# Optimization experiments

Measured on AMD Instinct MI355X. Metric: run time of the kernel, lower is better.

## Reference

```python
import jax, jax.numpy as jnp
import numpy as np

VOC_SIZE = 32768
DIM = 512
NUM_TOPK = 64
BATCH = 4096


def setup_inputs() -> dict:
    key = jax.random.key(0)
    ks = jax.random.split(key, 8)
    lim = 1.0 / np.sqrt(DIM)  # kaiming_uniform(a=sqrt(5)) on [V, d] -> U(-1/sqrt(d), 1/sqrt(d))
    x = jax.random.normal(ks[0], (BATCH, DIM), dtype=jnp.float32)
    codebook = jax.random.uniform(ks[1], (VOC_SIZE, DIM), dtype=jnp.float32, minval=-lim, maxval=lim)
    Wq = jax.random.uniform(ks[2], (DIM, DIM), dtype=jnp.float32, minval=-lim, maxval=lim)
    bq = jax.random.uniform(ks[3], (DIM,), dtype=jnp.float32, minval=-lim, maxval=lim)
    Wk = jax.random.uniform(ks[4], (DIM, DIM), dtype=jnp.float32, minval=-lim, maxval=lim)
    bk = jax.random.uniform(ks[5], (DIM,), dtype=jnp.float32, minval=-lim, maxval=lim)
    Wv = jax.random.uniform(ks[6], (DIM, DIM), dtype=jnp.float32, minval=-lim, maxval=lim)
    bv = jax.random.uniform(ks[7], (DIM,), dtype=jnp.float32, minval=-lim, maxval=lim)
    return {"x": x, "codebook": codebook, "Wq": Wq, "bq": bq,
            "Wk": Wk, "bk": bk, "Wv": Wv, "bv": bv}


def reference(x, codebook, Wq, bq, Wk, bk, Wv, bv):
    # projections (torch Linear with weight stored pre-transposed as [in, out])
    q = x @ Wq + bq              # [B, d]
    k = codebook @ Wk + bk       # [V, d]
    v = codebook @ Wv + bv       # [V, d]

    dots = jnp.einsum('bd,kd->bk', q, k)              # [B, V]
    top, _ = jax.lax.top_k(dots, NUM_TOPK)            # [B, num_topk]
    thresh = top[..., -1:]                            # k-th largest value per row
    mask_value = -jnp.finfo(dots.dtype).max
    dots = jnp.where(dots < thresh, mask_value, dots)
    attn = jax.nn.softmax(dots, axis=-1)              # [B, V]
    out = jnp.einsum('bk,kd->bd', attn, v)            # [B, d]
    return out
```

## Files before the change

### kernel.cpp

```cpp
#include <hip/hip_runtime.h>
#include <cstdint>

#define VOC   32768
#define DIM   512
#define TOPK  64
#define BATCH 4096

#define KSIG     2.45f
#define EPS_SEL  0.012f
#define CAND_CAP 512
#define RES_CAP  256
#define FCAP     1024

typedef unsigned short u16;
typedef __attribute__((ext_vector_type(8))) short bf16x8;
typedef __attribute__((ext_vector_type(4))) float f32x4;

__device__ __forceinline__ u16 f2bf(float f) {
    unsigned u = __float_as_uint(f);
    unsigned r = (u + 0x7FFFu + ((u >> 16) & 1u)) >> 16;
    return (u16)r;
}
__device__ __forceinline__ float bf2f(u16 h) {
    return __uint_as_float(((unsigned)h) << 16);
}
__device__ __forceinline__ unsigned enc16(u16 h) {
    return (h & 0x8000u) ? (unsigned)((u16)~h) : (unsigned)(h | 0x8000u);
}
__device__ __forceinline__ float dec16(unsigned s16) {
    u16 h = (s16 & 0x8000u) ? (u16)(s16 ^ 0x8000u) : (u16)(~s16);
    return bf2f(h);
}

__device__ __forceinline__ void async16(const void* g, void* l) {
    __builtin_amdgcn_global_load_lds(
        (const __attribute__((address_space(1))) void*)g,
        (__attribute__((address_space(3))) void*)l, 16, 0, 0);
}

template <bool BT, bool F64ACC>
__global__ __launch_bounds__(256)
void gemm64(const float* __restrict__ A, const float* __restrict__ B,
            const float* __restrict__ bias, float* __restrict__ C,
            int M, int N, int K)
{
    const int KS = 16;
    __shared__ float As[KS][68];
    __shared__ float Bs[KS][64];

    const int tid = threadIdx.x;
    const int m0 = blockIdx.y * 64;
    const int n0 = blockIdx.x * 64;
    const int ty = tid >> 4;
    const int tx = tid & 15;

    float acc[4][4];
    double acc64[4][4];
#pragma unroll
    for (int i = 0; i < 4; i++)
#pragma unroll
        for (int j = 0; j < 4; j++) { acc[i][j] = 0.f; if (F64ACC) acc64[i][j] = 0.0; }

    for (int kt = 0; kt < K; kt += KS) {
        {
            int row = tid >> 2, kq = tid & 3;
            const float4 av = *(const float4*)(A + (size_t)(m0 + row) * K + kt + kq * 4);
            As[kq * 4 + 0][row] = av.x;
            As[kq * 4 + 1][row] = av.y;
            As[kq * 4 + 2][row] = av.z;
            As[kq * 4 + 3][row] = av.w;
        }
        if (!BT) {
            int krow = tid >> 4, nq = tid & 15;
            *(float4*)&Bs[krow][nq * 4] =
                *(const float4*)(B + (size_t)(kt + krow) * N + n0 + nq * 4);
        } else {
            int nrow = tid >> 2, kq = tid & 3;
            const float4 bv = *(const float4*)(B + (size_t)(n0 + nrow) * K + kt + kq * 4);
            Bs[kq * 4 + 0][nrow] = bv.x;
            Bs[kq * 4 + 1][nrow] = bv.y;
            Bs[kq * 4 + 2][nrow] = bv.z;
            Bs[kq * 4 + 3][nrow] = bv.w;
        }
        __syncthreads();

#pragma unroll
        for (int kk = 0; kk < KS; kk++) {
            float4 a = *(const float4*)&As[kk][ty * 4];
            float4 b = *(const float4*)&Bs[kk][tx * 4];
            float av[4] = {a.x, a.y, a.z, a.w};
            float bv[4] = {b.x, b.y, b.z, b.w};
#pragma unroll
            for (int i = 0; i < 4; i++)
#pragma unroll
                for (int j = 0; j < 4; j++)
                    acc[i][j] += av[i] * bv[j];
        }
        __syncthreads();
        if (F64ACC) {
#pragma unroll
            for (int i = 0; i < 4; i++)
#pragma unroll
                for (int j = 0; j < 4; j++) { acc64[i][j] += (double)acc[i][j]; acc[i][j] = 0.f; }
        }
    }

    float4 bb = make_float4(0.f, 0.f, 0.f, 0.f);
    if (bias) bb = *(const float4*)(bias + n0 + tx * 4);
#pragma unroll
    for (int i = 0; i < 4; i++) {
        float4 o;
        o.x = (F64ACC ? (float)acc64[i][0] : acc[i][0]) + bb.x;
        o.y = (F64ACC ? (float)acc64[i][1] : acc[i][1]) + bb.y;
        o.z = (F64ACC ? (float)acc64[i][2] : acc[i][2]) + bb.z;
        o.w = (F64ACC ? (float)acc64[i][3] : acc[i][3]) + bb.w;
        *(float4*)(C + (size_t)(m0 + ty * 4 + i) * N + n0 + tx * 4) = o;
    }
}

__global__ __launch_bounds__(256)
void bias_fold(const float* __restrict__ bq, const float* __restrict__ Wk,
               float* __restrict__ bqk)
{
    const int lane = threadIdx.x & 63, wave = threadIdx.x >> 6;
    const int j = blockIdx.x * 4 + wave;
    const float* wr = Wk + (size_t)j * DIM + lane * 8;
    const float* bp = bq + lane * 8;
    double s = 0.0;
#pragma unroll
    for (int t = 0; t < 8; t++) s += (double)bp[t] * (double)wr[t];
#pragma unroll
    for (int off = 32; off > 0; off >>= 1) s += __shfl_down(s, off);
    if (lane == 0) bqk[j] = (float)s;
}

__global__ void zero_ws(unsigned* __restrict__ p, int n)
{
    int i = blockIdx.x * 256 + threadIdx.x;
    if (i < n) p[i] = 0u;
}

__global__ __launch_bounds__(256)
void cbar_accum(const float* __restrict__ cb, float* __restrict__ cbarsum)
{
    const int tid = threadIdx.x;
    const int r0 = blockIdx.x * 128;
    float s0 = 0.f, s1 = 0.f;
    for (int r = 0; r < 128; r++) {
        const float* rp = cb + (size_t)(r0 + r) * DIM;
        s0 += rp[tid];
        s1 += rp[tid + 256];
    }
    atomicAdd(&cbarsum[tid], s0);
    atomicAdd(&cbarsum[tid + 256], s1);
}

__global__ __launch_bounds__(256)
void rowstats(const float* __restrict__ q2, const float* __restrict__ cbarsum,
              float* __restrict__ trow, float* __restrict__ sigrow)
{
    const int tid = threadIdx.x, lane = tid & 63, wave = tid >> 6;
    const int row = blockIdx.x * 4 + wave;
    const float* qp = q2 + (size_t)row * DIM + lane * 8;
    float4 a0 = *(const float4*)qp, a1 = *(const float4*)(qp + 4);
    const float* cp = cbarsum + lane * 8;
    float4 c0 = *(const float4*)cp, c1 = *(const float4*)(cp + 4);
    float mu = a0.x*c0.x + a0.y*c0.y + a0.z*c0.z + a0.w*c0.w
             + a1.x*c1.x + a1.y*c1.y + a1.z*c1.z + a1.w*c1.w;
    float nr = a0.x*a0.x + a0.y*a0.y + a0.z*a0.z + a0.w*a0.w
             + a1.x*a1.x + a1.y*a1.y + a1.z*a1.z + a1.w*a1.w;
#pragma unroll
    for (int off = 32; off > 0; off >>= 1) {
        mu += __shfl_down(mu, off);
        nr += __shfl_down(nr, off);
    }
    if (lane == 0) {
        mu *= (1.f / VOC);
        float sig = sqrtf(nr * (1.f / 1536.f));
        trow[row] = mu + KSIG * sig;
        sigrow[row] = sig;
    }
}

__global__ __launch_bounds__(256)
void pack_rows(const float* __restrict__ src, u16* __restrict__ hi,
               u16* __restrict__ lo, int R, int log2R)
{
    int idx = blockIdx.x * 256 + threadIdx.x;
    int c8  = idx >> log2R;
    int row = idx & (R - 1);
    const float* sp = src + (size_t)row * DIM + c8 * 8;
    float xv[8];
    *(float4*)&xv[0] = *(const float4*)sp;
    *(float4*)&xv[4] = *(const float4*)(sp + 4);
    int ks = c8 >> 2, ch = c8 & 3;
    size_t ob = ((size_t)(ks * 4 + ch) * R + row) * 8;
    u16 h[8], l[8];
#pragma unroll
    for (int j = 0; j < 8; j++) {
        h[j] = f2bf(xv[j]);
        l[j] = f2bf(xv[j] - bf2f(h[j]));
    }
    *(uint4*)(hi + ob) = *(const uint4*)h;
    if (lo) *(uint4*)(lo + ob) = *(const uint4*)l;
}

__global__ __launch_bounds__(256)
void pack_bT(const float* __restrict__ W, u16* __restrict__ hi, u16* __restrict__ lo)
{
    int idx = blockIdx.x * 256 + threadIdx.x;
    int n  = idx & (DIM - 1);
    int c8 = idx >> 9;
    int ks = c8 >> 2, ch = c8 & 3;
    size_t ob = ((size_t)(ks * 4 + ch) * DIM + n) * 8;
    u16 h[8], l[8];
#pragma unroll
    for (int j = 0; j < 8; j++) {
        float x = W[(size_t)(c8 * 8 + j) * DIM + n];
        h[j] = f2bf(x);
        l[j] = f2bf(x - bf2f(h[j]));
    }
    *(uint4*)(hi + ob) = *(const uint4*)h;
    *(uint4*)(lo + ob) = *(const uint4*)l;
}

__global__ __launch_bounds__(256, 4)
void mfma_dots(const u16* __restrict__ Ah, const u16* __restrict__ Bh,
               const float* __restrict__ trow, unsigned* __restrict__ candBuf,
               unsigned* __restrict__ counters)
{
    __shared__ u16 lds[4 * 4096];

    const int tid  = threadIdx.x;
    const int lane = tid & 63;
    const int wave = tid >> 6;
    const int wm = wave >> 1, wn = wave & 1;
    const int lr = lane & 15;
    const int q  = lane >> 4;

    const int L   = blockIdx.x;
    const int xcd = L & 7;
    const int j   = L >> 3;
    const int m0  = (xcd * 4 + (j & 3)) * 128;
    const int n0  = (j >> 2) * 128;

    u16* wlds = &lds[wave * 4096];

#define AISSUE(ks, st)                                                         \
    { _Pragma("unroll")                                                        \
      for (int ch_ = 0; ch_ < 4; ch_++) {                                      \
          const u16* gp_ = Ah + ((size_t)((ks) * 4 + ch_) * BATCH              \
                                 + m0 + wm * 64 + lane) * 8;                   \
          async16(gp_, &wlds[(st) * 2048 + ch_ * 512 + lane * 8]);             \
      } }

#define BPTR(nt, ks) ((const bf16x8*)(Bh + ((size_t)((ks) * 4 + q) * VOC       \
                                            + n0 + wn * 64 + (nt) * 16 + lr) * 8))

    f32x4 acc[4][4] = {};
    bf16x8 bb[2][4];

    AISSUE(0, 0)
#pragma unroll
    for (int nt = 0; nt < 4; nt++) bb[0][nt] = *BPTR(nt, 0);

#pragma unroll
    for (int s = 0; s < 16; s++) {
        const int st = s & 1;
        __builtin_amdgcn_s_waitcnt(0x0F70);

        bf16x8 ah[4];
#pragma unroll
        for (int mt = 0; mt < 4; mt++)
            ah[mt] = *(const bf16x8*)&wlds[st * 2048 + q * 512 + (mt * 16 + lr) * 8];

        __builtin_amdgcn_sched_barrier(0);
        __builtin_amdgcn_s_waitcnt(0xC47F);
        if (s < 15) AISSUE(s + 1, st ^ 1)

        __builtin_amdgcn_s_setprio(1);
#pragma unroll
        for (int nt = 0; nt < 4; nt++) {
            if (s < 15) bb[st ^ 1][nt] = *BPTR(nt, s + 1);
#pragma unroll
            for (int mt = 0; mt < 4; mt++)
                acc[mt][nt] = __builtin_amdgcn_mfma_f32_16x16x32_bf16(
                    ah[mt], bb[st][nt], acc[mt][nt], 0, 0, 0);
        }
        __builtin_amdgcn_s_setprio(0);
    }
#undef AISSUE
#undef BPTR

#pragma unroll
    for (int mt = 0; mt < 4; mt++) {
#pragma unroll
        for (int r = 0; r < 4; r++) {
            int rowg = m0 + wm * 64 + mt * 16 + q * 4 + r;
            float tr = trow[rowg];
#pragma unroll
            for (int nt = 0; nt < 4; nt++) {
                float val = acc[mt][nt][r];
                if (val >= tr) {
                    unsigned slot = atomicAdd(&counters[rowg], 1u);
                    if (slot < CAND_CAP) {
                        unsigned s16 = enc16(f2bf(val));
                        candBuf[(size_t)rowg * CAND_CAP + slot] =
                            (s16 << 16) | (unsigned)(n0 + wn * 64 + nt * 16 + lr);
                    }
                }
            }
        }
    }
}

__global__ __launch_bounds__(256, 2)
void mfma_out(const u16* __restrict__ Ah, const u16* __restrict__ Al,
              const u16* __restrict__ Bh, const u16* __restrict__ Bl,
              const float* __restrict__ bias, float* __restrict__ Cout, int Ma)
{
    __shared__ u16 lds[2 * 16384];

    const int tid  = threadIdx.x;
    const int lane = tid & 63;
    const int wave = tid >> 6;
    const int wm = wave >> 1, wn = wave & 1;
    const int m0 = blockIdx.y * 128, n0 = blockIdx.x * 128;
    const int lr = lane & 15;
    const int q  = lane >> 4;

    f32x4 acc[4][4] = {};
    const u16* garr[4] = {Ah, Bh, Al, Bl};
    const int a = wave;
    const u16* src = garr[a];
    const bool isA = (a == 0 || a == 2);
    const int rb = isA ? m0 : n0;
    const size_t R = isA ? (size_t)Ma : (size_t)DIM;

#define VISSUE(ks, b)                                                         \
    {                                                                         \
        _Pragma("unroll")                                                     \
        for (int i_ = 0; i_ < 8; i_++) {                                      \
            const u16* gp_ = src + ((size_t)((ks) * 4 + (i_ >> 1)) * R + rb   \
                                    + (i_ & 1) * 64 + lane) * 8;              \
            async16(gp_, &lds[(b) * 16384 + a * 4096 + i_ * 512 + lane * 8]); \
        }                                                                     \
    }

    VISSUE(0, 0)

    for (int ks = 0; ks < 16; ks++) {
        __syncthreads();
        if (ks < 15) VISSUE(ks + 1, (ks + 1) & 1)
        const u16* base = &lds[(ks & 1) * 16384];

        bf16x8 ah[4], al[4];
#pragma unroll
        for (int mt = 0; mt < 4; mt++) {
            int row = wm * 64 + mt * 16 + lr;
            ah[mt] = *(const bf16x8*)&base[0 * 4096 + q * 1024 + row * 8];
            al[mt] = *(const bf16x8*)&base[2 * 4096 + q * 1024 + row * 8];
        }
#pragma unroll
        for (int nt = 0; nt < 4; nt++) {
            int col = wn * 64 + nt * 16 + lr;
            bf16x8 bh = *(const bf16x8*)&base[1 * 4096 + q * 1024 + col * 8];
            bf16x8 bl = *(const bf16x8*)&base[3 * 4096 + q * 1024 + col * 8];
#pragma unroll
            for (int mt = 0; mt < 4; mt++) {
                acc[mt][nt] = __builtin_amdgcn_mfma_f32_16x16x32_bf16(ah[mt], bh, acc[mt][nt], 0, 0, 0);
                acc[mt][nt] = __builtin_amdgcn_mfma_f32_16x16x32_bf16(ah[mt], bl, acc[mt][nt], 0, 0, 0);
                acc[mt][nt] = __builtin_amdgcn_mfma_f32_16x16x32_bf16(al[mt], bh, acc[mt][nt], 0, 0, 0);
            }
        }
    }
#undef VISSUE

#pragma unroll
    for (int mt = 0; mt < 4; mt++)
#pragma unroll
        for (int nt = 0; nt < 4; nt++) {
            int col = n0 + wn * 64 + nt * 16 + lr;
            float bb = bias[col];
#pragma unroll
            for (int r = 0; r < 4; r++) {
                int rowg = m0 + wm * 64 + mt * 16 + q * 4 + r;
                Cout[(size_t)rowg * DIM + col] = acc[mt][nt][r] + bb;
            }
        }
}

__global__ __launch_bounds__(256)
void select6(const unsigned* __restrict__ candBuf, const unsigned* __restrict__ counters,
             const float* __restrict__ trow, const float* __restrict__ q2,
             const float* __restrict__ codebook, float* __restrict__ y,
             unsigned* __restrict__ flags)
{
    __shared__ unsigned recs[CAND_CAP];
    __shared__ unsigned list[RES_CAP];
    __shared__ unsigned hist[256];
    __shared__ unsigned long long keys[RES_CAP];
    __shared__ float q2s[DIM];
    __shared__ float wArr[RES_CAP];
    __shared__ float redf[256];
    __shared__ unsigned redu[256];
    __shared__ unsigned s_R;
    __shared__ unsigned s_b1, s_rem, s_thr;

    const int tid  = threadIdx.x;
    const int lane = tid & 63;
    const int wave = tid >> 6;
    const int row  = blockIdx.x;

    const unsigned cnt = counters[row];
    if (cnt < TOPK || cnt > CAND_CAP) {
        if (tid == 0) flags[row] = 1u;
        return;
    }
    for (int i = tid; i < DIM; i += 256) q2s[i] = q2[(size_t)row * DIM + i];
    for (int i = tid; i < CAND_CAP; i += 256)
        recs[i] = (i < (int)cnt) ? candBuf[(size_t)row * CAND_CAP + i] : 0u;
    if (tid == 0) s_R = 0;
    hist[tid] = 0;
    __syncthreads();

#pragma unroll
    for (int e = 0; e < 2; e++) {
        int i = tid + e * 256;
        if (i < (int)cnt) atomicAdd(&hist[recs[i] >> 24], 1u);
    }
    __syncthreads();
    if (tid == 0) {
        unsigned c = 0; int b = 255;
        for (; b > 0; b--) {
            unsigned h = hist[b];
            if (c + h >= TOPK) break;
            c += h;
        }
        s_b1 = (unsigned)b; s_rem = TOPK - c;
    }
    __syncthreads();
    const unsigned b1 = s_b1, rem = s_rem;
    hist[tid] = 0;
    __syncthreads();

#pragma unroll
    for (int e = 0; e < 2; e++) {
        int i = tid + e * 256;
        if (i < (int)cnt && (recs[i] >> 24) == b1)
            atomicAdd(&hist[(recs[i] >> 16) & 0xFFu], 1u);
    }
    __syncthreads();
    if (tid == 0) {
        unsigned c = 0; int b = 255;
        for (; b > 0; b--) {
            unsigned h = hist[b];
            if (c + h >= rem) break;
            c += h;
        }
        s_thr = (b1 << 8) | (unsigned)b;
    }
    __syncthreads();

    const float a64  = dec16(s_thr);
    const float band = a64 - 2.f * EPS_SEL;
    if (trow[row] > band) {
        if (tid == 0) flags[row] = 1u;
        return;
    }

#pragma unroll
    for (int e = 0; e < 2; e++) {
        int i = tid + e * 256;
        if (i < (int)cnt && dec16(recs[i] >> 16) >= band) {
            unsigned p = atomicAdd(&s_R, 1u);
            if (p < RES_CAP) list[p] = recs[i];
        }
    }
    __syncthreads();
    const int R = (int)s_R;
    if (R > RES_CAP) {
        if (tid == 0) flags[row] = 1u;
        return;
    }

    for (int c = wave; c < R; c += 4) {
        unsigned idx = list[c] & 0xFFFFu;
        const float* cb = codebook + (size_t)idx * DIM + lane * 8;
        float4 c0 = *(const float4*)cb, c1 = *(const float4*)(cb + 4);
        const float* qp = &q2s[lane * 8];
        float4 a0 = *(const float4*)qp, a1 = *(const float4*)(qp + 4);
        double s = (double)a0.x * c0.x + (double)a0.y * c0.y
                 + (double)a0.z * c0.z + (double)a0.w * c0.w
                 + (double)a1.x * c1.x + (double)a1.y * c1.y
                 + (double)a1.z * c1.z + (double)a1.w * c1.w;
#pragma unroll
        for (int off = 32; off > 0; off >>= 1) s += __shfl_down(s, off);
        if (lane == 0) {
            float val = (float)s;
            unsigned b = __float_as_uint(val);
            unsigned sk = (b & 0x80000000u) ? ~b : (b | 0x80000000u);
            keys[c] = ((unsigned long long)(~sk) << 32) | idx;
        }
    }
    if (tid >= R && tid < RES_CAP) keys[tid] = ~0ULL;
    __syncthreads();

    for (int k = 2; k <= RES_CAP; k <<= 1) {
        for (int j = k >> 1; j > 0; j >>= 1) {
            int ixj = tid ^ j;
            if (ixj > tid) {
                unsigned long long a = keys[tid], b2 = keys[ixj];
                if (((tid & k) == 0) ? (a > b2) : (a < b2)) { keys[tid] = b2; keys[ixj] = a; }
            }
            __syncthreads();
        }
    }

    const unsigned threshInv = (unsigned)(keys[TOPK - 1] >> 32);
    unsigned sk0 = ~(unsigned)(keys[0] >> 32);
    const float vmax = __uint_as_float((sk0 & 0x80000000u) ? (sk0 & 0x7FFFFFFFu) : ~sk0);

    unsigned hi = (unsigned)(keys[tid] >> 32);
    bool sel = (hi <= threshInv);
    unsigned sk = ~hi;
    float val = __uint_as_float((sk & 0x80000000u) ? (sk & 0x7FFFFFFFu) : ~sk);
    float w = sel ? expf(val - vmax) : 0.f;
    wArr[tid] = w;
    redf[tid] = w;
    redu[tid] = sel ? 1u : 0u;
    __syncthreads();
    for (int s = 128; s > 0; s >>= 1) {
        if (tid < s) { redf[tid] += redf[tid + s]; redu[tid] += redu[tid + s]; }
        __syncthreads();
    }
    const float invZ = 1.0f / redf[0];
    const int selCount = (int)redu[0];

    for (int d = tid; d < DIM; d += 256) {
        float acc = 0.f;
        for (int i = 0; i < selCount; i++) {
            unsigned idx = (unsigned)(keys[i] & 0xFFFFFFFFu);
            acc += wArr[i] * codebook[(size_t)idx * DIM + d];
        }
        y[(size_t)row * DIM + d] = acc * invZ;
    }
}

__global__ __launch_bounds__(256)
void fallback_row(const unsigned* __restrict__ flags, const float* __restrict__ q2,
                  const float* __restrict__ codebook, const float* __restrict__ trow,
                  const float* __restrict__ sigrow, float* __restrict__ y)
{
    const int row = blockIdx.x;
    if (!flags[row]) return;

    __shared__ float q2s[DIM];
    __shared__ unsigned long long keys[FCAP];
    __shared__ float wArr[FCAP];
    __shared__ float redf[256];
    __shared__ unsigned redu[256];
    __shared__ unsigned s_cnt;

    const int tid = threadIdx.x;
    for (int i = tid; i < DIM; i += 256) q2s[i] = q2[(size_t)row * DIM + i];
    const float sig = sigrow[row];
    float tf = trow[row] - 0.35f * sig;
    unsigned cnt = 0;

    for (int it = 0; it < 16; it++) {
        if (tid == 0) s_cnt = 0;
        __syncthreads();
        for (int i = tid; i < VOC; i += 256) {
            const float* cb = codebook + (size_t)i * DIM;
            double s = 0.0;
            for (int d = 0; d < DIM; d += 4) {
                float4 c4 = *(const float4*)(cb + d);
                s += (double)q2s[d + 0] * (double)c4.x + (double)q2s[d + 1] * (double)c4.y
                   + (double)q2s[d + 2] * (double)c4.z + (double)q2s[d + 3] * (double)c4.w;
            }
            float vv = (float)s;
            if (vv >= tf) {
                unsigned p = atomicAdd(&s_cnt, 1u);
                if (p < FCAP) {
                    unsigned b = __float_as_uint(vv);
                    unsigned sk = (b & 0x80000000u) ? ~b : (b | 0x80000000u);
                    keys[p] = ((unsigned long long)(~sk) << 32) | (unsigned)i;
                }
            }
        }
        __syncthreads();
        cnt = s_cnt;
        if (cnt > FCAP) { tf += 0.15f * sig; continue; }
        if (cnt < TOPK) { tf -= 0.35f * sig; continue; }
        break;
    }
    if (cnt > FCAP) cnt = FCAP;
    for (int i = tid; i < FCAP; i += 256)
        if (i >= (int)cnt) keys[i] = ~0ULL;
    __syncthreads();

    for (int k = 2; k <= FCAP; k <<= 1) {
        for (int j = k >> 1; j > 0; j >>= 1) {
#pragma unroll
            for (int e = 0; e < 4; e++) {
                int i = tid + e * 256;
                int ixj = i ^ j;
                if (ixj > i) {
                    unsigned long long a = keys[i], b = keys[ixj];
                    if (((i & k) == 0) ? (a > b) : (a < b)) { keys[i] = b; keys[ixj] = a; }
                }
            }
            __syncthreads();
        }
    }

    const unsigned threshInv = (unsigned)(keys[TOPK - 1] >> 32);
    unsigned sk0 = ~(unsigned)(keys[0] >> 32);
    const float vmax = __uint_as_float((sk0 & 0x80000000u) ? (sk0 & 0x7FFFFFFFu) : ~sk0);

    float lsum = 0.f; unsigned lcnt = 0;
    for (int i = tid; i < FCAP; i += 256) {
        unsigned hi = (unsigned)(keys[i] >> 32);
        bool sel = (hi <= threshInv);
        unsigned sk = ~hi;
        float vv = __uint_as_float((sk & 0x80000000u) ? (sk & 0x7FFFFFFFu) : ~sk);
        float w = sel ? expf(vv - vmax) : 0.f;
        wArr[i] = w;
        lsum += w; lcnt += sel ? 1u : 0u;
    }
    redf[tid] = lsum; redu[tid] = lcnt;
    __syncthreads();
    for (int s = 128; s > 0; s >>= 1) {
        if (tid < s) { redf[tid] += redf[tid + s]; redu[tid] += redu[tid + s]; }
        __syncthreads();
    }
    const float invZ = 1.f / redf[0];
    const int selCount = (int)redu[0];

    for (int d = tid; d < DIM; d += 256) {
        float acc = 0.f;
        for (int i = 0; i < selCount; i++) {
            unsigned idx = (unsigned)(keys[i] & 0xFFFFFFFFu);
            acc += wArr[i] * codebook[(size_t)idx * DIM + d];
        }
        y[(size_t)row * DIM + d] = acc * invZ;
    }
}

extern "C" void kernel_launch(void* const* d_in, const int* in_sizes, int n_in,
                              void* d_out, int out_size, void* d_ws, size_t ws_size,
                              hipStream_t stream)
{
    const float* x        = (const float*)d_in[0];
    const float* codebook = (const float*)d_in[1];
    const float* Wq       = (const float*)d_in[2];
    const float* bq       = (const float*)d_in[3];
    const float* Wk       = (const float*)d_in[4];
    const float* Wv       = (const float*)d_in[6];
    const float* bv       = (const float*)d_in[7];
    float* out = (float*)d_out;

    float* q2   = (float*)d_ws;
    float* Wqk  = q2   + (size_t)BATCH * DIM;
    float* bqk  = Wqk  + (size_t)DIM * DIM;
    float* y    = bqk  + 1024;
    float* trow = y    + (size_t)BATCH * DIM;
    float* sigr = trow + BATCH;
    unsigned* counters = (unsigned*)(sigr + BATCH);
    unsigned* flags    = counters + BATCH;
    float* cbarsum     = (float*)(flags + BATCH);
    unsigned* candBuf  = (unsigned*)(cbarsum + 512);
    u16* q2h = (u16*)(candBuf + (size_t)BATCH * CAND_CAP);
    u16* cbh = q2h + (size_t)BATCH * DIM;
    u16* yh  = cbh + (size_t)VOC * DIM;
    u16* yl  = yh  + (size_t)BATCH * DIM;
    u16* wvh = yl  + (size_t)BATCH * DIM;
    u16* wvl = wvh + (size_t)DIM * DIM;

    u16* xh   = yh;
    u16* xl   = yl;
    u16* wqkh = (u16*)candBuf;
    u16* wqkl = wqkh + (size_t)DIM * DIM;

    dim3 blk(256);

    gemm64<true, true><<<dim3(DIM / 64, DIM / 64), blk, 0, stream>>>(
        Wq, Wk, nullptr, Wqk, DIM, DIM, DIM);
    bias_fold<<<dim3(DIM / 4), blk, 0, stream>>>(bq, Wk, bqk);

    pack_bT<<<dim3(DIM * 64 / 256), blk, 0, stream>>>(Wqk, wqkh, wqkl);
    pack_rows<<<dim3(BATCH * 64 / 256), blk, 0, stream>>>(x, xh, xl, BATCH, 12);
    mfma_out<<<dim3(DIM / 128, BATCH / 128), blk, 0, stream>>>(
        xh, xl, wqkh, wqkl, bqk, q2, BATCH);

    zero_ws<<<dim3(34), blk, 0, stream>>>(counters, BATCH * 2 + 512);

    cbar_accum<<<dim3(VOC / 128), blk, 0, stream>>>(codebook, cbarsum);
    rowstats<<<dim3(BATCH / 4), blk, 0, stream>>>(q2, cbarsum, trow, sigr);

    pack_rows<<<dim3(BATCH * 64 / 256), blk, 0, stream>>>(q2, q2h, nullptr, BATCH, 12);
    pack_rows<<<dim3(VOC * 64 / 256), blk, 0, stream>>>(codebook, cbh, nullptr, VOC, 15);
    pack_bT<<<dim3(DIM * 64 / 256), blk, 0, stream>>>(Wv, wvh, wvl);

    mfma_dots<<<dim3(8192), blk, 0, stream>>>(q2h, cbh, trow, candBuf, counters);

    select6<<<dim3(BATCH), blk, 0, stream>>>(
        candBuf, counters, trow, q2, codebook, y, flags);
    fallback_row<<<dim3(BATCH), blk, 0, stream>>>(
        flags, q2, codebook, trow, sigr, y);

    pack_rows<<<dim3(BATCH * 64 / 256), blk, 0, stream>>>(y, yh, yl, BATCH, 12);
    mfma_out<<<dim3(DIM / 128, BATCH / 128), blk, 0, stream>>>(
        yh, yl, wvh, wvl, bv, out, BATCH);
}
```

Measured before the change: 689.7 us.

## Enlarge mfma_dots block tile to 256x128 with shared LDS staging of A and B

The dots GEMM block grows from 256 to 512 threads (8 waves) and covers a 256x128 tile. Both the A (query) and B (codebook) slices are now staged asynchronously into double-buffered LDS, with a block barrier each k-step. Previously each wave loaded only its own A slice into private LDS and read B straight from global memory into registers. The change aims to share B across waves and raise reuse per global byte, at the cost of block-wide barriers and loss of the per-wave register prefetch of B.

Result: slower. 1.515 ms (+119.7%).

```diff
diff --git a/kernel.cpp b/kernel.cpp
--- a/kernel.cpp
+++ b/kernel.cpp
@@ -224,12 +224,12 @@
     *(uint4*)(lo + ob) = *(const uint4*)l;
 }
 
-__global__ __launch_bounds__(256, 4)
+__global__ __launch_bounds__(512, 6)
 void mfma_dots(const u16* __restrict__ Ah, const u16* __restrict__ Bh,
                const float* __restrict__ trow, unsigned* __restrict__ candBuf,
                unsigned* __restrict__ counters)
 {
-    __shared__ u16 lds[4 * 4096];
+    __shared__ u16 lds[2 * 12288];
 
     const int tid  = threadIdx.x;
     const int lane = tid & 63;
@@ -241,56 +241,49 @@
     const int L   = blockIdx.x;
     const int xcd = L & 7;
     const int j   = L >> 3;
-    const int m0  = (xcd * 4 + (j & 3)) * 128;
-    const int n0  = (j >> 2) * 128;
-
-    u16* wlds = &lds[wave * 4096];
-
-#define AISSUE(ks, st)                                                         \
-    { _Pragma("unroll")                                                        \
-      for (int ch_ = 0; ch_ < 4; ch_++) {                                      \
-          const u16* gp_ = Ah + ((size_t)((ks) * 4 + ch_) * BATCH              \
-                                 + m0 + wm * 64 + lane) * 8;                   \
-          async16(gp_, &wlds[(st) * 2048 + ch_ * 512 + lane * 8]);             \
-      } }
-
-#define BPTR(nt, ks) ((const bf16x8*)(Bh + ((size_t)((ks) * 4 + q) * VOC       \
-                                            + n0 + wn * 64 + (nt) * 16 + lr) * 8))
+    const int m0  = (xcd * 2 + (j & 1)) * 256;
+    const int n0  = (j >> 1) * 128;
+
+    const size_t stepA = (size_t)4 * BATCH * 8;
+    const size_t stepB = (size_t)4 * VOC * 8;
+    const int uA0 = tid, uA1 = tid + 512;
+    const u16* gA0 = Ah + ((size_t)(uA0 >> 8) * BATCH + m0 + (uA0 & 255)) * 8;
+    const u16* gA1 = Ah + ((size_t)(uA1 >> 8) * BATCH + m0 + (uA1 & 255)) * 8;
+    const u16* gB  = Bh + ((size_t)(tid >> 7) * VOC + n0 + (tid & 127)) * 8;
+    const int lA0 = uA0 * 8, lA1 = uA1 * 8, lB = 8192 + tid * 8;
+
+#define ISSUE(b)                                                              \
+    {                                                                         \
+        async16(gA0, &lds[(b) * 12288 + lA0]); gA0 += stepA;                  \
+        async16(gA1, &lds[(b) * 12288 + lA1]); gA1 += stepA;                  \
+        async16(gB,  &lds[(b) * 12288 + lB ]); gB  += stepB;                  \
+    }
 
     f32x4 acc[4][4] = {};
-    bf16x8 bb[2][4];
-
-    AISSUE(0, 0)
-#pragma unroll
-    for (int nt = 0; nt < 4; nt++) bb[0][nt] = *BPTR(nt, 0);
-
-#pragma unroll
+
+    ISSUE(0)
+
     for (int s = 0; s < 16; s++) {
-        const int st = s & 1;
         __builtin_amdgcn_s_waitcnt(0x0F70);
+        __builtin_amdgcn_s_barrier();
+        if (s < 15) ISSUE((s + 1) & 1)
+        const u16* base = &lds[(s & 1) * 12288];
 
         bf16x8 ah[4];
 #pragma unroll
         for (int mt = 0; mt < 4; mt++)
-            ah[mt] = *(const bf16x8*)&wlds[st * 2048 + q * 512 + (mt * 16 + lr) * 8];
-
-        __builtin_amdgcn_sched_barrier(0);
-        __builtin_amdgcn_s_waitcnt(0xC47F);
-        if (s < 15) AISSUE(s + 1, st ^ 1)
-
+            ah[mt] = *(const bf16x8*)&base[q * 2048 + (wm * 64 + mt * 16 + lr) * 8];
         __builtin_amdgcn_s_setprio(1);
 #pragma unroll
         for (int nt = 0; nt < 4; nt++) {
-            if (s < 15) bb[st ^ 1][nt] = *BPTR(nt, s + 1);
+            bf16x8 bh = *(const bf16x8*)&base[8192 + q * 1024 + (wn * 64 + nt * 16 + lr) * 8];
 #pragma unroll
             for (int mt = 0; mt < 4; mt++)
-                acc[mt][nt] = __builtin_amdgcn_mfma_f32_16x16x32_bf16(
-                    ah[mt], bb[st][nt], acc[mt][nt], 0, 0, 0);
+                acc[mt][nt] = __builtin_amdgcn_mfma_f32_16x16x32_bf16(ah[mt], bh, acc[mt][nt], 0, 0, 0);
         }
         __builtin_amdgcn_s_setprio(0);
     }
-#undef AISSUE
-#undef BPTR
+#undef ISSUE
 
 #pragma unroll
     for (int mt = 0; mt < 4; mt++) {
@@ -703,7 +696,7 @@
     pack_rows<<<dim3(VOC * 64 / 256), blk, 0, stream>>>(codebook, cbh, nullptr, VOC, 15);
     pack_bT<<<dim3(DIM * 64 / 256), blk, 0, stream>>>(Wv, wvh, wvl);
 
-    mfma_dots<<<dim3(8192), blk, 0, stream>>>(q2h, cbh, trow, candBuf, counters);
+    mfma_dots<<<dim3(4096), dim3(512), 0, stream>>>(q2h, cbh, trow, candBuf, counters);
 
     select6<<<dim3(BATCH), blk, 0, stream>>>(
         candBuf, counters, trow, q2, codebook, y, flags);
```
